# Optimization experiments

Measured on AMD Instinct MI355X. Metric: run time of the kernel, lower is better.

Reference implementation:

```python
import jax, jax.numpy as jnp
import numpy as np

B, S, D = 2, 2048, 2048
H, KVH, HD = 32, 8, 64
GROUPS = H // KVH  # 4
NEG = -1e9


def setup_inputs() -> dict:
    key = jax.random.key(0)
    ks = jax.random.split(key, 5)
    x = jax.random.normal(ks[0], (B, S, D), dtype=jnp.float32)
    # causal additive mask [1,1,S,S]
    causal = jnp.triu(jnp.full((S, S), NEG, dtype=jnp.float32), k=1)[None, None]
    Wq = jax.random.normal(ks[1], (D, D), dtype=jnp.float32) * (D ** -0.5)
    Wk = jax.random.normal(ks[2], (KVH * HD, D), dtype=jnp.float32) * (D ** -0.5)
    Wv = jax.random.normal(ks[3], (KVH * HD, D), dtype=jnp.float32) * (D ** -0.5)
    Wo = jax.random.normal(ks[4], (D, D), dtype=jnp.float32) * (D ** -0.5)
    return {"x": x, "attention_mask": causal, "Wq": Wq, "Wk": Wk, "Wv": Wv, "Wo": Wo}


def reference(x, attention_mask, Wq, Wk, Wv, Wo):
    b, s, _ = x.shape
    # projections (nn.Linear: y = x @ W.T)
    q = (x @ Wq.T).reshape(b, s, H, HD).transpose(0, 2, 1, 3)      # [b,H,s,hd]
    k = (x @ Wk.T).reshape(b, s, KVH, HD).transpose(0, 2, 1, 3)    # [b,KVH,s,hd]
    v = (x @ Wv.T).reshape(b, s, KVH, HD).transpose(0, 2, 1, 3)
    new_kv_cache = (k, v)
    # repeat_interleave over head dim for GQA
    k = jnp.repeat(k, GROUPS, axis=1)  # [b,H,s,hd]
    v = jnp.repeat(v, GROUPS, axis=1)
    scale = 1.0 / jnp.sqrt(jnp.float32(HD))
    scores = jnp.einsum('bhqd,bhkd->bhqk', q, k) * scale
    scores = scores + attention_mask
    attn = jax.nn.softmax(scores.astype(jnp.float32), axis=-1).astype(q.dtype)
    out = jnp.einsum('bhqk,bhkd->bhqd', attn, v)  # [b,H,s,hd]
    out = out.transpose(0, 2, 1, 3).reshape(b, s, H * HD)
    output = out @ Wo.T
    return (output, new_kv_cache[0], new_kv_cache[1])
```

## Files before the change

kernel.cpp:

```cpp
#include <hip/hip_runtime.h>
#include <hip/hip_bf16.h>
#include <stdint.h>

#define B_ 2
#define S_ 2048
#define D_ 2048
#define H_ 32
#define KVH_ 8
#define HD_ 64

typedef __bf16 bf16x8 __attribute__((ext_vector_type(8)));
typedef float f32x4 __attribute__((ext_vector_type(4)));

#define MFMA16(a, b, c) __builtin_amdgcn_mfma_f32_16x16x32_bf16((a), (b), (c), 0, 0, 0)

typedef __attribute__((address_space(1))) void gvoid_t;
typedef __attribute__((address_space(3))) void lvoid_t;

__device__ __forceinline__ void async_ld16(__hip_bfloat16* lds, const __hip_bfloat16* g) {
  __builtin_amdgcn_global_load_lds((gvoid_t*)(void*)(g), (lvoid_t*)(lds), 16, 0, 0);
}

__device__ __forceinline__ unsigned short f2bu(float f) {
  __hip_bfloat16 h = __float2bfloat16(f);
  return *reinterpret_cast<unsigned short*>(&h);
}

__global__ void cast_all_kernel(const float* __restrict__ x,
                                const float* __restrict__ wq,
                                const float* __restrict__ wk,
                                const float* __restrict__ wv,
                                const float* __restrict__ wo,
                                unsigned short* __restrict__ xb,
                                unsigned short* __restrict__ wqkvb,
                                unsigned short* __restrict__ wob) {
  constexpr int NX = B_ * S_ * D_ / 4;
  constexpr int NQ = D_ * D_ / 4;
  constexpr int NK = KVH_ * HD_ * D_ / 4;
  constexpr int E0 = NX;
  constexpr int E1 = E0 + NQ;
  constexpr int E2 = E1 + NK;
  constexpr int E3 = E2 + NK;
  constexpr int E4 = E3 + NQ;
  const int stride = gridDim.x * blockDim.x;
  for (int i = blockIdx.x * blockDim.x + threadIdx.x; i < E4; i += stride) {
    const float* src; unsigned short* dst; int j;
    if (i < E0)      { src = x;  dst = xb;                              j = i; }
    else if (i < E1) { src = wq; dst = wqkvb;                           j = i - E0; }
    else if (i < E2) { src = wk; dst = wqkvb + (size_t)2048 * D_;       j = i - E1; }
    else if (i < E3) { src = wv; dst = wqkvb + (size_t)2560 * D_;       j = i - E2; }
    else             { src = wo; dst = wob;                             j = i - E3; }
    float4 v = reinterpret_cast<const float4*>(src)[j];
    ushort4 o;
    o.x = f2bu(v.x); o.y = f2bu(v.y); o.z = f2bu(v.z); o.w = f2bu(v.w);
    reinterpret_cast<ushort4*>(dst)[j] = o;
  }
}

template <int MODE>
__global__ __launch_bounds__(256, 2)
void gemm_bt(const __hip_bfloat16* __restrict__ A,
             const __hip_bfloat16* __restrict__ W,
             float* __restrict__ Cf, __hip_bfloat16* __restrict__ Cb,
             float* __restrict__ Cf2, __hip_bfloat16* __restrict__ Cb2,
             __hip_bfloat16* __restrict__ Cb3,
             int M, int N, int K) {
  __shared__ __align__(16) __hip_bfloat16 sA[128 * 32];
  __shared__ __align__(16) __hip_bfloat16 sB[128 * 32];
  const int tid = threadIdx.x;
  const int lane = tid & 63;
  const int wv = tid >> 6;
  const int l15 = lane & 15, l4 = lane >> 4;
  const int bm = blockIdx.x * 128, bn = blockIdx.y * 128;
  const int wm = (wv >> 1) * 64, wn = (wv & 1) * 64;

  const int ci0 = tid, ci1 = tid + 256;
  const __hip_bfloat16* gA0 = A + (size_t)(bm + (ci0 >> 2)) * K + (ci0 & 3) * 8;
  const __hip_bfloat16* gA1 = A + (size_t)(bm + (ci1 >> 2)) * K + (ci1 & 3) * 8;
  const __hip_bfloat16* gB0 = W + (size_t)(bn + (ci0 >> 2)) * K + (ci0 & 3) * 8;
  const __hip_bfloat16* gB1 = W + (size_t)(bn + (ci1 >> 2)) * K + (ci1 & 3) * 8;
  __hip_bfloat16* lA0 = &sA[ci0 * 8];
  __hip_bfloat16* lA1 = &sA[ci1 * 8];
  __hip_bfloat16* lB0 = &sB[ci0 * 8];
  __hip_bfloat16* lB1 = &sB[ci1 * 8];

  f32x4 acc[4][4];
#pragma unroll
  for (int i = 0; i < 4; ++i) {
#pragma unroll
    for (int j = 0; j < 4; ++j) acc[i][j] = f32x4{0.f, 0.f, 0.f, 0.f};
  }

  for (int k0 = 0; k0 < K; k0 += 32) {
    async_ld16(lA0, gA0 + k0);
    async_ld16(lA1, gA1 + k0);
    async_ld16(lB0, gB0 + k0);
    async_ld16(lB1, gB1 + k0);
    __syncthreads();
    bf16x8 af[4], bfr[4];
#pragma unroll
    for (int i = 0; i < 4; ++i)
      af[i] = *reinterpret_cast<const bf16x8*>(&sA[(wm + i * 16 + l15) * 32 + l4 * 8]);
#pragma unroll
    for (int j = 0; j < 4; ++j)
      bfr[j] = *reinterpret_cast<const bf16x8*>(&sB[(wn + j * 16 + l15) * 32 + l4 * 8]);
#pragma unroll
    for (int i = 0; i < 4; ++i) {
#pragma unroll
      for (int j = 0; j < 4; ++j) acc[i][j] = MFMA16(af[i], bfr[j], acc[i][j]);
    }
    __syncthreads();
  }

#pragma unroll
  for (int i = 0; i < 4; ++i) {
#pragma unroll
    for (int j = 0; j < 4; ++j) {
      const int col = bn + wn + j * 16 + l15;
#pragma unroll
      for (int r = 0; r < 4; ++r) {
        const int row = bm + wm + i * 16 + l4 * 4 + r;
        const float v = acc[i][j][r];
        if (MODE == 1) {
          Cf[(size_t)row * N + col] = v;
        } else {
          if (bn < 2048) {
            Cb[(size_t)row * 2048 + col] = __float2bfloat16(v);
          } else {
            const int bb = row >> 11, s = row & 2047;
            const int kv = col - 2048;
            if (kv < 512) {
              const int g = kv >> 6, hd = kv & 63;
              const size_t idx = ((size_t)(bb * KVH_ + g) * S_ + s) * HD_ + hd;
              Cf[idx] = v;
              Cb2[idx] = __float2bfloat16(v);
            } else {
              const int vv = kv - 512;
              const int g = vv >> 6, hd = vv & 63;
              const size_t idx = ((size_t)(bb * KVH_ + g) * S_ + s) * HD_ + hd;
              Cf2[idx] = v;
              Cb3[((size_t)(bb * KVH_ + g) * HD_ + hd) * S_ + s] = __float2bfloat16(v);
            }
          }
        }
      }
    }
  }
}

__global__ __launch_bounds__(512, 4)
void attn_fused(const __hip_bfloat16* __restrict__ Qb,
                const __hip_bfloat16* __restrict__ Kb,
                const __hip_bfloat16* __restrict__ Vtb,
                __hip_bfloat16* __restrict__ AOb) {
  __shared__ __align__(16) __hip_bfloat16 sK[2][64 * 64];
  __shared__ __align__(16) __hip_bfloat16 sV[2][64 * 64];
  __shared__ __align__(16) __hip_bfloat16 sP[8 * 16 * 64];

  const int tid = threadIdx.x;
  const int lane = tid & 63;
  const int wv = tid >> 6;
  const int l15 = lane & 15, l4 = lane >> 4;
  const int h = blockIdx.x & 31;
  const int b = blockIdx.x >> 5;
  const int qt = 15 - blockIdx.y;
  const int g = h >> 2;

  bf16x8 qf[2];
  {
    const __hip_bfloat16* Qp =
        Qb + ((size_t)(b * S_ + qt * 128 + wv * 16 + l15)) * D_ + h * HD_;
#pragma unroll
    for (int c = 0; c < 2; ++c)
      qf[c] = *reinterpret_cast<const bf16x8*>(Qp + c * 32 + l4 * 8);
  }

  f32x4 oacc[4];
  f32x4 lacc = f32x4{0.f, 0.f, 0.f, 0.f};
#pragma unroll
  for (int j = 0; j < 4; ++j) oacc[j] = f32x4{0.f, 0.f, 0.f, 0.f};

  bf16x8 vone;
#pragma unroll
  for (int j = 0; j < 8; ++j) vone[j] = (__bf16)1.0f;

  const __hip_bfloat16* Kp = Kb + (size_t)(b * KVH_ + g) * S_ * HD_;
  const __hip_bfloat16* Vp = Vtb + (size_t)(b * KVH_ + g) * HD_ * S_;
  __hip_bfloat16* sPw = sP + wv * (16 * 64);
  const float CE = 0.125f * 1.4426950408889634f;
  const float MSUB = 8.0f;

  const int r0 = tid >> 3, c0 = (tid & 7) ^ (r0 & 7);
  const __hip_bfloat16* gk = Kp + (size_t)r0 * HD_ + c0 * 8;
  const __hip_bfloat16* gv = Vp + (size_t)r0 * S_ + c0 * 8;

  auto stage = [&](int buf) {
    async_ld16(&sK[buf][tid * 8], gk);
    async_ld16(&sV[buf][tid * 8], gv);
    gk += 64 * HD_;
    gv += 64;
  };

  auto pack = [&](f32x4 (&sc)[4], int koff) {
    if (koff >= 0) {
#pragma unroll
      for (int jn = 0; jn < 4; ++jn) {
        const int kp = koff + jn * 16 + l15;
#pragma unroll
        for (int r = 0; r < 4; ++r) {
          const int qp = wv * 16 + l4 * 4 + r;
          if (kp > qp) sc[jn][r] = -3.0e38f;
        }
      }
    }
#pragma unroll
    for (int jj = 0; jj < 4; ++jj) {
#pragma unroll
      for (int r = 0; r < 4; ++r) {
        const float p = exp2f(fmaf(sc[jj][r], CE, -MSUB));
        sPw[(l4 * 4 + r) * 64 + ((jj ^ l4) * 16 + l15)] = __float2bfloat16(p);
      }
    }
  };

  const int nsteps = 2 * qt + 2;
  stage(0);
  for (int ki = 0; ki < nsteps; ++ki) {
    const int cur = ki & 1;
    __syncthreads();
    if (ki + 1 < nsteps) stage(cur ^ 1);
    const int ko = ((ki >> 1) == qt) ? (ki & 1) * 64 : -1;

    f32x4 sc[4];
    __builtin_amdgcn_s_setprio(1);
#pragma unroll
    for (int jn = 0; jn < 4; ++jn) {
      const int row = jn * 16 + l15;
      const bf16x8 k0 = *reinterpret_cast<const bf16x8*>(
          &sK[cur][(row * 8 + (l4 ^ (row & 7))) * 8]);
      const bf16x8 k1 = *reinterpret_cast<const bf16x8*>(
          &sK[cur][(row * 8 + ((4 + l4) ^ (row & 7))) * 8]);
      f32x4 t = f32x4{0.f, 0.f, 0.f, 0.f};
      t = MFMA16(qf[0], k0, t);
      t = MFMA16(qf[1], k1, t);
      sc[jn] = t;
    }
    __builtin_amdgcn_s_setprio(0);

    pack(sc, ko);

    const int gr = (l15 >> 2) & 3;
    __builtin_amdgcn_s_setprio(1);
#pragma unroll
    for (int kc = 0; kc < 2; ++kc) {
      bf16x8 vf[4];
#pragma unroll
      for (int jn = 0; jn < 4; ++jn) {
        const int row = jn * 16 + l15;
        vf[jn] = *reinterpret_cast<const bf16x8*>(
            &sV[cur][(row * 8 + ((kc * 4 + l4) ^ (row & 7))) * 8]);
      }
      const int pcol = (((kc * 2 + (l4 >> 1)) ^ gr) * 16 + (l4 & 1) * 8);
      const bf16x8 pf = *reinterpret_cast<const bf16x8*>(&sPw[l15 * 64 + pcol]);
#pragma unroll
      for (int jn = 0; jn < 4; ++jn) oacc[jn] = MFMA16(pf, vf[jn], oacc[jn]);
      lacc = MFMA16(pf, vone, lacc);
    }
    __builtin_amdgcn_s_setprio(0);
  }

  float inv[4];
#pragma unroll
  for (int r = 0; r < 4; ++r) inv[r] = 1.0f / lacc[r];
#pragma unroll
  for (int jn = 0; jn < 4; ++jn) {
#pragma unroll
    for (int r = 0; r < 4; ++r) {
      const int qp = qt * 128 + wv * 16 + l4 * 4 + r;
      AOb[(size_t)(b * S_ + qp) * D_ + h * HD_ + jn * 16 + l15] =
          __float2bfloat16(oacc[jn][r] * inv[r]);
    }
  }
}

extern "C" void kernel_launch(void* const* d_in, const int* in_sizes, int n_in,
                              void* d_out, int out_size, void* d_ws, size_t ws_size,
                              hipStream_t stream) {
  (void)in_sizes; (void)n_in; (void)out_size; (void)ws_size;
  const float* x = (const float*)d_in[0];
  const float* Wq = (const float*)d_in[2];
  const float* Wk = (const float*)d_in[3];
  const float* Wv = (const float*)d_in[4];
  const float* Wo = (const float*)d_in[5];

  float* outO = (float*)d_out;
  float* outK = outO + (size_t)B_ * S_ * D_;
  float* outV = outK + (size_t)B_ * KVH_ * S_ * HD_;

  char* p = (char*)d_ws;
  __hip_bfloat16* xb    = (__hip_bfloat16*)p; p += (size_t)B_ * S_ * D_ * 2;
  __hip_bfloat16* Wqkvb = (__hip_bfloat16*)p; p += (size_t)3072 * D_ * 2;
  __hip_bfloat16* Wob   = (__hip_bfloat16*)p; p += (size_t)D_ * D_ * 2;
  __hip_bfloat16* Qbf   = (__hip_bfloat16*)p; p += (size_t)B_ * S_ * D_ * 2;
  __hip_bfloat16* Kbf   = (__hip_bfloat16*)p; p += (size_t)B_ * KVH_ * S_ * HD_ * 2;
  __hip_bfloat16* Vtb   = (__hip_bfloat16*)p; p += (size_t)B_ * KVH_ * S_ * HD_ * 2;
  __hip_bfloat16* AOb   = (__hip_bfloat16*)p; p += (size_t)B_ * S_ * D_ * 2;

  cast_all_kernel<<<dim3(4096), dim3(256), 0, stream>>>(
      x, Wq, Wk, Wv, Wo,
      (unsigned short*)xb, (unsigned short*)Wqkvb, (unsigned short*)Wob);

  gemm_bt<4><<<dim3(32, 24), dim3(256), 0, stream>>>(
      xb, Wqkvb, outK, Qbf, outV, Kbf, Vtb, 4096, 3072, 2048);
  attn_fused<<<dim3(64, 16, 1), dim3(512), 0, stream>>>(Qbf, Kbf, Vtb, AOb);
  gemm_bt<1><<<dim3(32, 16), dim3(256), 0, stream>>>(
      AOb, Wob, outO, nullptr, nullptr, nullptr, nullptr, 4096, 2048, 2048);
}
```

Baseline: 308.7 us.

## Double GEMM K-tile to 64, XOR-swizzle LDS layout, and remap workgroups

The bf16 GEMM now stages a 64-wide K slice per iteration instead of 32, which halves the number of barriers per unit of work. LDS chunks are XOR-swizzled by row so that MFMA fragment reads avoid bank conflicts, with the matching permutation applied on the global-address side. Workgroup ids are remapped so that neighbouring blocks run on different XCD groups and share A/W tiles in cache. The cost is twice the LDS per block, which may limit occupancy under launch bounds of 2 blocks per CU, and the loads are still not double-buffered.

```diff
diff --git a/kernel.cpp b/kernel.cpp
--- a/kernel.cpp
+++ b/kernel.cpp
@@ -65,24 +65,31 @@
              float* __restrict__ Cf2, __hip_bfloat16* __restrict__ Cb2,
              __hip_bfloat16* __restrict__ Cb3,
              int M, int N, int K) {
-  __shared__ __align__(16) __hip_bfloat16 sA[128 * 32];
-  __shared__ __align__(16) __hip_bfloat16 sB[128 * 32];
+  __shared__ __align__(16) __hip_bfloat16 sA[128 * 64];
+  __shared__ __align__(16) __hip_bfloat16 sB[128 * 64];
   const int tid = threadIdx.x;
   const int lane = tid & 63;
   const int wv = tid >> 6;
   const int l15 = lane & 15, l4 = lane >> 4;
-  const int bm = blockIdx.x * 128, bn = blockIdx.y * 128;
+
+  const int nwg = gridDim.x * gridDim.y;
+  const int lid = blockIdx.y * gridDim.x + blockIdx.x;
+  const int swz = (lid & 7) * (nwg >> 3) + (lid >> 3);
+  const int bm = (swz % gridDim.x) * 128;
+  const int bn = (swz / gridDim.x) * 128;
+
   const int wm = (wv >> 1) * 64, wn = (wv & 1) * 64;
 
-  const int ci0 = tid, ci1 = tid + 256;
-  const __hip_bfloat16* gA0 = A + (size_t)(bm + (ci0 >> 2)) * K + (ci0 & 3) * 8;
-  const __hip_bfloat16* gA1 = A + (size_t)(bm + (ci1 >> 2)) * K + (ci1 & 3) * 8;
-  const __hip_bfloat16* gB0 = W + (size_t)(bn + (ci0 >> 2)) * K + (ci0 & 3) * 8;
-  const __hip_bfloat16* gB1 = W + (size_t)(bn + (ci1 >> 2)) * K + (ci1 & 3) * 8;
-  __hip_bfloat16* lA0 = &sA[ci0 * 8];
-  __hip_bfloat16* lA1 = &sA[ci1 * 8];
-  __hip_bfloat16* lB0 = &sB[ci0 * 8];
-  __hip_bfloat16* lB1 = &sB[ci1 * 8];
+  const __hip_bfloat16* gA[4];
+  const __hip_bfloat16* gB[4];
+#pragma unroll
+  for (int i = 0; i < 4; ++i) {
+    const int ci = tid + i * 256;
+    const int row = ci >> 3;
+    const int lc = (ci & 7) ^ (row & 7);
+    gA[i] = A + (size_t)(bm + row) * K + lc * 8;
+    gB[i] = W + (size_t)(bn + row) * K + lc * 8;
+  }
 
   f32x4 acc[4][4];
 #pragma unroll
@@ -91,23 +98,33 @@
     for (int j = 0; j < 4; ++j) acc[i][j] = f32x4{0.f, 0.f, 0.f, 0.f};
   }
 
-  for (int k0 = 0; k0 < K; k0 += 32) {
-    async_ld16(lA0, gA0 + k0);
-    async_ld16(lA1, gA1 + k0);
-    async_ld16(lB0, gB0 + k0);
-    async_ld16(lB1, gB1 + k0);
+  for (int k0 = 0; k0 < K; k0 += 64) {
+#pragma unroll
+    for (int i = 0; i < 4; ++i) {
+      async_ld16(&sA[(tid + i * 256) * 8], gA[i] + k0);
+      async_ld16(&sB[(tid + i * 256) * 8], gB[i] + k0);
+    }
     __syncthreads();
-    bf16x8 af[4], bfr[4];
-#pragma unroll
-    for (int i = 0; i < 4; ++i)
-      af[i] = *reinterpret_cast<const bf16x8*>(&sA[(wm + i * 16 + l15) * 32 + l4 * 8]);
-#pragma unroll
-    for (int j = 0; j < 4; ++j)
-      bfr[j] = *reinterpret_cast<const bf16x8*>(&sB[(wn + j * 16 + l15) * 32 + l4 * 8]);
-#pragma unroll
-    for (int i = 0; i < 4; ++i) {
-#pragma unroll
-      for (int j = 0; j < 4; ++j) acc[i][j] = MFMA16(af[i], bfr[j], acc[i][j]);
+#pragma unroll
+    for (int kk = 0; kk < 2; ++kk) {
+      bf16x8 af[4], bfr[4];
+#pragma unroll
+      for (int i = 0; i < 4; ++i) {
+        const int row = wm + i * 16 + l15;
+        af[i] = *reinterpret_cast<const bf16x8*>(
+            &sA[row * 64 + (((kk * 4 + l4) ^ (row & 7)) * 8)]);
+      }
+#pragma unroll
+      for (int j = 0; j < 4; ++j) {
+        const int row = wn + j * 16 + l15;
+        bfr[j] = *reinterpret_cast<const bf16x8*>(
+            &sB[row * 64 + (((kk * 4 + l4) ^ (row & 7)) * 8)]);
+      }
+#pragma unroll
+      for (int i = 0; i < 4; ++i) {
+#pragma unroll
+        for (int j = 0; j < 4; ++j) acc[i][j] = MFMA16(af[i], bfr[j], acc[i][j]);
+      }
     }
     __syncthreads();
   }
```

Measured after the change: 312.1 us. Within noise of the previous version (+1.1%).
